# Performance work log

Measured on AMD Instinct MI355X. Metric: run time of the kernel, lower is better.

Reference implementation:

```python
import jax, jax.numpy as jnp
import numpy as np

B = 32; L = 512; D_MODEL = 512; N_LAYERS = 4
D_STATE = 64; D_CONV = 4; EXPAND = 2; HEADDIM = 64; PRED = 96
D_INNER = EXPAND * D_MODEL            # 1024
NHEADS = D_INNER // HEADDIM           # 16
CONV_DIM = D_INNER + 2 * D_STATE      # 1152
D_IN_PROJ = 2 * D_INNER + 2 * D_STATE + NHEADS  # 2192
EPS = 1e-5


def setup_inputs() -> dict:
    key = jax.random.key(0)
    ks = jax.random.split(key, 8)
    s = lambda k, shape, scale=0.02: jax.random.normal(k, shape, jnp.float32) * scale
    return {
        "x": jax.random.normal(ks[0], (B, L, D_MODEL), jnp.float32),
        "in_proj_w": s(ks[1], (N_LAYERS, D_IN_PROJ, D_MODEL)),
        "conv_w": s(ks[2], (N_LAYERS, CONV_DIM, D_CONV), 0.2),
        "conv_b": jnp.zeros((N_LAYERS, CONV_DIM), jnp.float32),
        "dt_bias": jnp.log(jnp.expm1(jax.random.uniform(ks[3], (N_LAYERS, NHEADS), minval=0.001, maxval=0.1))),
        "A_log": jnp.log(jax.random.uniform(ks[4], (N_LAYERS, NHEADS), minval=1.0, maxval=16.0)),
        "Dp": jnp.ones((N_LAYERS, NHEADS), jnp.float32),
        "norm_w": jnp.ones((N_LAYERS, D_INNER), jnp.float32),
        "out_proj_w": s(ks[5], (N_LAYERS, D_MODEL, D_INNER)),
        "ln_w": jnp.ones((N_LAYERS, D_MODEL), jnp.float32),
        "ln_b": jnp.zeros((N_LAYERS, D_MODEL), jnp.float32),
        "final_w": s(ks[6], (D_MODEL, D_MODEL)),
        "final_b": jnp.zeros((D_MODEL,), jnp.float32),
    }


def _silu(x):
    return x * jax.nn.sigmoid(x)


def _causal_dwconv(x, w, b):
    # x: (B, L, C); depthwise causal conv, kernel D_CONV, left pad D_CONV-1
    xt = jnp.swapaxes(x, 1, 2)  # (B, C, L)
    y = jax.lax.conv_general_dilated(
        xt, w[:, None, :], window_strides=(1,), padding=[(D_CONV - 1, 0)],
        feature_group_count=CONV_DIM, dimension_numbers=("NCH", "OIH", "NCH"))
    return jnp.swapaxes(y + b[None, :, None], 1, 2)


def _ssd_scan(xh, dt, Bm, Cm, A, Dp):
    # xh: (B,L,H,P), dt: (B,L,H), Bm/Cm: (B,L,N), A/Dp: (H,)
    dA = jnp.exp(dt * A)  # (B,L,H)

    def step(h, t):
        dA_t, x_t, dt_t, B_t, C_t = t  # (B,H), (B,H,P), (B,H), (B,N), (B,N)
        h = h * dA_t[:, :, None, None] + (dt_t[:, :, None] * x_t)[..., None] * B_t[:, None, None, :]
        y = jnp.einsum("bhpn,bn->bhp", h, C_t)
        return h, y

    Bb, Ll, H, P = xh.shape
    N = Bm.shape[-1]
    h0 = jnp.zeros((Bb, H, P, N), xh.dtype)
    xs = (jnp.moveaxis(dA, 1, 0), jnp.moveaxis(xh, 1, 0), jnp.moveaxis(dt, 1, 0),
          jnp.moveaxis(Bm, 1, 0), jnp.moveaxis(Cm, 1, 0))
    _, ys = jax.lax.scan(step, h0, xs)
    y = jnp.moveaxis(ys, 0, 1)  # (B,L,H,P)
    return y + xh * Dp[None, None, :, None]


def _mamba2(x, w_in, cw, cb, dtb, a_log, dp, nw, w_out):
    zxbcdt = jnp.einsum("bld,ed->ble", x, w_in)  # (B,L,D_IN_PROJ)
    z = zxbcdt[..., :D_INNER]
    xBC = zxbcdt[..., D_INNER:D_INNER + CONV_DIM]
    dt = jax.nn.softplus(zxbcdt[..., -NHEADS:] + dtb)
    xBC = _silu(_causal_dwconv(xBC, cw, cb))
    xh = xBC[..., :D_INNER].reshape(x.shape[0], x.shape[1], NHEADS, HEADDIM)
    Bm = xBC[..., D_INNER:D_INNER + D_STATE]
    Cm = xBC[..., D_INNER + D_STATE:]
    A = -jnp.exp(a_log)
    y = _ssd_scan(xh, dt, Bm, Cm, A, dp).reshape(x.shape[0], x.shape[1], D_INNER)
    # gated RMSNorm (norm_before_gate=False): gate first, then normalize
    y = y * _silu(z)
    y = y * jax.lax.rsqrt(jnp.mean(y * y, axis=-1, keepdims=True) + EPS) * nw
    return jnp.einsum("ble,de->bld", y, w_out)


def _layernorm(x, w, b):
    xc = x - jnp.mean(x, axis=-1, keepdims=True)
    return xc * jax.lax.rsqrt(jnp.mean(xc * xc, axis=-1, keepdims=True) + EPS) * w + b


def reference(x, in_proj_w, conv_w, conv_b, dt_bias, A_log, Dp, norm_w,
              out_proj_w, ln_w, ln_b, final_w, final_b):
    h = x
    for i in range(N_LAYERS):
        res = h
        h = _mamba2(h, in_proj_w[i], conv_w[i], conv_b[i], dt_bias[i],
                    A_log[i], Dp[i], norm_w[i], out_proj_w[i])
        h = _layernorm(h + res, ln_w[i], ln_b[i])
        # dropout is identity in eval mode
    h = h[:, -PRED:, :]
    return jnp.einsum("bld,ed->ble", h, final_w) + final_b
```

## Files before the change

### kernel.cpp

```cpp
#include <hip/hip_runtime.h>
#include <stdint.h>

#define BATCH 32
#define SEQ   512
#define DM    512
#define NL    4
#define DSTATE 64
#define DI    1024
#define NH    16
#define HD    64
#define PREDN 96
#define CDIM  1152
#define CSEG  144
#define DPROJ 2192
#define XBW   1168
#define NC    8
#define EPSF  1e-5f

typedef float  f32x4  __attribute__((ext_vector_type(4)));
typedef __bf16 bf16x4 __attribute__((ext_vector_type(4)));
typedef __bf16 bf16x8 __attribute__((ext_vector_type(8)));

__device__ __forceinline__ float sigmoidf_(float x){ return 1.f/(1.f+__expf(-x)); }
__device__ __forceinline__ float siluf_(float x){ return x*sigmoidf_(x); }
__device__ __forceinline__ float softplusf_(float x){ return (x>20.f)?x:log1pf(__expf(x)); }

__device__ __forceinline__ void gld16(const void* g, void* l){
  __builtin_amdgcn_global_load_lds((__attribute__((address_space(1))) void*)g,
                                   (__attribute__((address_space(3))) void*)l, 16, 0, 0);
}

template<typename TC>
__global__ __launch_bounds__(256) void gemm128(
    const __bf16* __restrict__ A, const __bf16* __restrict__ W,
    TC* __restrict__ C, TC* __restrict__ C2, const float* __restrict__ bias,
    int M, int Nreal, int ldc, int ldc2, int splitN, int K)
{
  __shared__ __bf16 sA[128*64];
  __shared__ __bf16 sW[128*64];
  const int tid  = threadIdx.x;
  const int m0   = blockIdx.y*128, n0 = blockIdx.x*128;
  const int lane = tid&63, wave = tid>>6;
  const int l15  = lane&15, quad = lane>>4;
  const int wr   = (wave>>1)*64, wc = (wave&1)*64;
  f32x4 acc[4][4];
  #pragma unroll
  for (int a=0;a<4;++a)
    #pragma unroll
    for (int b=0;b<4;++b) acc[a][b] = (f32x4){0,0,0,0};

  for (int k0=0; k0<K; k0+=64){
    #pragma unroll
    for (int j=0;j<4;++j){
      const int f = j*256 + tid;
      const int r = f>>3;
      const int kc = (((f&7) ^ (r&7)))*8;
      gld16(A + (size_t)(m0+r)*K + k0 + kc, &sA[f*8]);
      int rb = n0 + r; rb = rb < Nreal ? rb : (Nreal-1);
      gld16(W + (size_t)rb*K + k0 + kc, &sW[f*8]);
    }
    __syncthreads();
    #pragma unroll
    for (int kk=0; kk<64; kk+=32){
      const int kcb = (kk>>3) + quad;
      bf16x8 av[4], bv[4];
      #pragma unroll
      for (int mi=0;mi<4;++mi){
        const int row = wr+mi*16+l15;
        av[mi] = *(const bf16x8*)&sA[row*64 + ((kcb ^ (row&7))<<3)];
      }
      #pragma unroll
      for (int ni=0;ni<4;++ni){
        const int row = wc+ni*16+l15;
        bv[ni] = *(const bf16x8*)&sW[row*64 + ((kcb ^ (row&7))<<3)];
      }
      #pragma unroll
      for (int mi=0;mi<4;++mi)
        #pragma unroll
        for (int ni=0;ni<4;++ni)
          acc[mi][ni] = __builtin_amdgcn_mfma_f32_16x16x32_bf16(av[mi],bv[ni],acc[mi][ni],0,0,0);
    }
    __syncthreads();
  }
  #pragma unroll
  for (int ni=0;ni<4;++ni){
    const int col = n0 + wc + ni*16 + l15;
    if (col < Nreal){
      const float badd = bias ? bias[col] : 0.f;
      #pragma unroll
      for (int mi=0;mi<4;++mi){
        #pragma unroll
        for (int r4=0;r4<4;++r4){
          const int row = m0 + wr + mi*16 + quad*4 + r4;
          const float v = acc[mi][ni][r4] + badd;
          if (col < splitN) C [(size_t)row*ldc  + col]          = (TC)v;
          else              C2[(size_t)row*ldc2 + (col-splitN)] = (TC)v;
        }
      }
    }
  }
}

__global__ __launch_bounds__(256) void cast_bf16_k(
    const float* __restrict__ src, __bf16* __restrict__ dst, int n4)
{
  int i = blockIdx.x*256 + threadIdx.x;
  if (i < n4){
    float4 v = ((const float4*)src)[i];
    bf16x4 o;
    o[0]=(__bf16)v.x; o[1]=(__bf16)v.y; o[2]=(__bf16)v.z; o[3]=(__bf16)v.w;
    ((bf16x4*)dst)[i] = o;
  }
}

__global__ __launch_bounds__(256) void conv_silu_k(
    const __bf16* __restrict__ xbw, const float* __restrict__ cw,
    const float* __restrict__ cb, __bf16* __restrict__ xout,
    __bf16* __restrict__ bcout)
{
  int idx = blockIdx.x*256 + threadIdx.x;
  if (idx >= BATCH*SEQ*CSEG) return;
  const int seg = idx % CSEG;
  const int bt  = idx / CSEG;
  const int t = bt % SEQ, b = bt / SEQ;
  const int d0 = seg*8;
  const __bf16* src = xbw + ((size_t)b*SEQ + t)*XBW + d0;
  bf16x8 z8;
  #pragma unroll
  for (int e=0;e<8;++e) z8[e]=(__bf16)0.f;
  bf16x8 x3 = *(const bf16x8*)src;
  bf16x8 x2 = (t>=1)? *(const bf16x8*)(src -   XBW) : z8;
  bf16x8 x1 = (t>=2)? *(const bf16x8*)(src - 2*XBW) : z8;
  bf16x8 x0 = (t>=3)? *(const bf16x8*)(src - 3*XBW) : z8;
  const float4* w4  = (const float4*)(cw + (size_t)d0*4);
  const float4* cb4 = (const float4*)(cb + d0);
  float4 cbl = cb4[0], cbh = cb4[1];
  bf16x8 o;
  #pragma unroll
  for (int e=0;e<8;++e){
    float4 w = w4[e];
    float acc = (e<4 ? (&cbl.x)[e] : (&cbh.x)[e-4])
              + w.x*(float)x0[e] + w.y*(float)x1[e]
              + w.z*(float)x2[e] + w.w*(float)x3[e];
    o[e] = (__bf16)siluf_(acc);
  }
  if (d0 < DI) *(bf16x8*)(xout  + ((size_t)b*SEQ+t)*DI  + d0)       = o;
  else         *(bf16x8*)(bcout + ((size_t)b*SEQ+t)*128 + (d0-DI))  = o;
}

__global__ __launch_bounds__(256) void ssd_fused_k(
    const __bf16* __restrict__ bc,
    __bf16* __restrict__ xy,
    const __bf16* __restrict__ xbw,
    const float* __restrict__ dtb_, const float* __restrict__ alog_,
    const float* __restrict__ dp_)
{
  __shared__ __bf16 sB[64*72], sC[64*72], sXT[64*72], sBwT[64*72],
                    sS[64*72], sHT[64*72];
  __shared__ float sCS[SEQ], sDT[SEQ];
  const int bid = blockIdx.x;
  const int h = bid & 15, b = bid >> 4;
  const int tid = threadIdx.x, wave = tid>>6, lane = tid&63;
  const int l15 = lane&15, quad = lane>>4;
  const int wm = (wave>>1)*32, wn = (wave&1)*32;

  const float Ah  = -__expf(alog_[h]);
  const float dtb = dtb_[h];
  const float Dh  = dp_[h];

  for (int t = tid; t < SEQ; t += 256){
    float raw = (float)xbw[((size_t)b*SEQ + t)*XBW + CDIM + h];
    float dt = softplusf_(raw + dtb);
    sDT[t] = dt;
    sCS[t] = dt*Ah;
  }
  __syncthreads();
  for (int ch = wave; ch < NC; ch += 4){
    float s = sCS[ch*64 + lane];
    #pragma unroll
    for (int off=1; off<64; off<<=1){
      float v = __shfl_up(s, off);
      if (lane >= off) s += v;
    }
    sCS[ch*64 + lane] = s;
  }
  __syncthreads();

  f32x4 run[2][2];
  #pragma unroll
  for (int a=0;a<2;++a)
    #pragma unroll
    for (int d=0;d<2;++d) run[a][d] = (f32x4){0,0,0,0};

  for (int c = 0; c < NC; ++c){
    const int t0 = c*64;
    {
      const int r = tid>>2, seg = (tid&3)*16;
      const __bf16* row = bc + ((size_t)b*SEQ + t0 + r)*128;
      bf16x8 vb0 = *(const bf16x8*)(row + seg);
      bf16x8 vb1 = *(const bf16x8*)(row + seg + 8);
      bf16x8 vc0 = *(const bf16x8*)(row + 64 + seg);
      bf16x8 vc1 = *(const bf16x8*)(row + 64 + seg + 8);
      *(bf16x8*)&sB[r*72+seg]   = vb0;
      *(bf16x8*)&sB[r*72+seg+8] = vb1;
      *(bf16x8*)&sC[r*72+seg]   = vc0;
      *(bf16x8*)&sC[r*72+seg+8] = vc1;
      const float w = __expf(sCS[t0+63] - sCS[t0+r]) * sDT[t0+r];
      #pragma unroll
      for (int e=0;e<8;++e){
        sBwT[(seg+e)*72 + r]   = (__bf16)(w*(float)vb0[e]);
        sBwT[(seg+8+e)*72 + r] = (__bf16)(w*(float)vb1[e]);
      }
      const __bf16* xrow = xy + ((size_t)b*SEQ + t0 + r)*DI + h*64;
      bf16x8 vx0 = *(const bf16x8*)(xrow + seg);
      bf16x8 vx1 = *(const bf16x8*)(xrow + seg + 8);
      #pragma unroll
      for (int e=0;e<8;++e){
        sXT[(seg+e)*72 + r]   = vx0[e];
        sXT[(seg+8+e)*72 + r] = vx1[e];
      }
    }
    __syncthreads();

    f32x4 aS[2][2];
    #pragma unroll
    for (int a=0;a<2;++a)
      #pragma unroll
      for (int d=0;d<2;++d) aS[a][d] = (f32x4){0,0,0,0};
    #pragma unroll
    for (int kk=0; kk<64; kk+=32){
      const int kf = kk + quad*8;
      bf16x8 a0 = *(const bf16x8*)&sC[(wm+l15)*72+kf];
      bf16x8 a1 = *(const bf16x8*)&sC[(wm+16+l15)*72+kf];
      bf16x8 b0 = *(const bf16x8*)&sB[(wn+l15)*72+kf];
      bf16x8 b1 = *(const bf16x8*)&sB[(wn+16+l15)*72+kf];
      aS[0][0] = __builtin_amdgcn_mfma_f32_16x16x32_bf16(a0,b0,aS[0][0],0,0,0);
      aS[0][1] = __builtin_amdgcn_mfma_f32_16x16x32_bf16(a0,b1,aS[0][1],0,0,0);
      aS[1][0] = __builtin_amdgcn_mfma_f32_16x16x32_bf16(a1,b0,aS[1][0],0,0,0);
      aS[1][1] = __builtin_amdgcn_mfma_f32_16x16x32_bf16(a1,b1,aS[1][1],0,0,0);
    }
    #pragma unroll
    for (int mi=0;mi<2;++mi)
      #pragma unroll
      for (int ni=0;ni<2;++ni)
        #pragma unroll
        for (int r4=0;r4<4;++r4){
          const int i = wm+mi*16+quad*4+r4, j = wn+ni*16+l15;
          float ed = __expf(fminf(sCS[t0+i]-sCS[t0+j], 0.f)) * sDT[t0+j];
          float v = aS[mi][ni][r4]*ed;
          sS[i*72+j] = (__bf16)((j<=i)? v : 0.f);
          sHT[j*72+i] = (__bf16)run[mi][ni][r4];
        }
    __syncthreads();

    f32x4 aY[2][2], aH[2][2], aYi[2][2];
    #pragma unroll
    for (int a=0;a<2;++a)
      #pragma unroll
      for (int d=0;d<2;++d){
        aY[a][d]=(f32x4){0,0,0,0}; aH[a][d]=(f32x4){0,0,0,0};
        aYi[a][d]=(f32x4){0,0,0,0};
      }
    #pragma unroll
    for (int kk=0; kk<64; kk+=32){
      const int kf = kk + quad*8;
      bf16x8 b0 = *(const bf16x8*)&sXT[(wn+l15)*72+kf];
      bf16x8 b1 = *(const bf16x8*)&sXT[(wn+16+l15)*72+kf];
      bf16x8 s0 = *(const bf16x8*)&sS[(wm+l15)*72+kf];
      bf16x8 s1 = *(const bf16x8*)&sS[(wm+16+l15)*72+kf];
      bf16x8 w0 = *(const bf16x8*)&sBwT[(wm+l15)*72+kf];
      bf16x8 w1 = *(const bf16x8*)&sBwT[(wm+16+l15)*72+kf];
      bf16x8 c0 = *(const bf16x8*)&sC[(wm+l15)*72+kf];
      bf16x8 c1 = *(const bf16x8*)&sC[(wm+16+l15)*72+kf];
      bf16x8 h0 = *(const bf16x8*)&sHT[(wn+l15)*72+kf];
      bf16x8 h1 = *(const bf16x8*)&sHT[(wn+16+l15)*72+kf];
      aY[0][0] = __builtin_amdgcn_mfma_f32_16x16x32_bf16(s0,b0,aY[0][0],0,0,0);
      aY[0][1] = __builtin_amdgcn_mfma_f32_16x16x32_bf16(s0,b1,aY[0][1],0,0,0);
      aY[1][0] = __builtin_amdgcn_mfma_f32_16x16x32_bf16(s1,b0,aY[1][0],0,0,0);
      aY[1][1] = __builtin_amdgcn_mfma_f32_16x16x32_bf16(s1,b1,aY[1][1],0,0,0);
      aH[0][0] = __builtin_amdgcn_mfma_f32_16x16x32_bf16(w0,b0,aH[0][0],0,0,0);
      aH[0][1] = __builtin_amdgcn_mfma_f32_16x16x32_bf16(w0,b1,aH[0][1],0,0,0);
      aH[1][0] = __builtin_amdgcn_mfma_f32_16x16x32_bf16(w1,b0,aH[1][0],0,0,0);
      aH[1][1] = __builtin_amdgcn_mfma_f32_16x16x32_bf16(w1,b1,aH[1][1],0,0,0);
      aYi[0][0] = __builtin_amdgcn_mfma_f32_16x16x32_bf16(c0,h0,aYi[0][0],0,0,0);
      aYi[0][1] = __builtin_amdgcn_mfma_f32_16x16x32_bf16(c0,h1,aYi[0][1],0,0,0);
      aYi[1][0] = __builtin_amdgcn_mfma_f32_16x16x32_bf16(c1,h0,aYi[1][0],0,0,0);
      aYi[1][1] = __builtin_amdgcn_mfma_f32_16x16x32_bf16(c1,h1,aYi[1][1],0,0,0);
    }

    const float lam = __expf(sCS[t0+63]);
    #pragma unroll
    for (int mi=0;mi<2;++mi)
      #pragma unroll
      for (int ni=0;ni<2;++ni)
        #pragma unroll
        for (int r4=0;r4<4;++r4){
          const int i = wm+mi*16+quad*4+r4;
          const int p = wn+ni*16+l15;
          const float xval = (float)sXT[p*72 + i];
          const float e2 = __expf(sCS[t0+i]);
          const float yv = aY[mi][ni][r4] + Dh*xval + e2*aYi[mi][ni][r4];
          xy[((size_t)b*SEQ + t0 + i)*DI + h*64 + p] = (__bf16)yv;
          run[mi][ni][r4] = run[mi][ni][r4]*lam + aH[mi][ni][r4];
        }
    __syncthreads();
  }
}

__global__ __launch_bounds__(256) void gate_rms_k(
    __bf16* __restrict__ y, const __bf16* __restrict__ z, const float* __restrict__ nw)
{
  __shared__ float red[4];
  const int tid = threadIdx.x;
  const int sub = tid>>7;
  const int off = (tid&127)*8;
  const size_t row = (size_t)blockIdx.x*2 + sub;
  __bf16* yrow = y + row*DI;
  const __bf16* zrow = z + row*DI;
  bf16x8 yv = *(const bf16x8*)(yrow+off);
  bf16x8 zv = *(const bf16x8*)(zrow+off);
  float u[8]; float ss = 0.f;
  #pragma unroll
  for (int e=0;e<8;++e){
    float uu = (float)yv[e]*siluf_((float)zv[e]);
    u[e]=uu; ss += uu*uu;
  }
  #pragma unroll
  for (int o=32;o;o>>=1) ss += __shfl_xor(ss,o);
  if ((tid&63)==0) red[tid>>6] = ss;
  __syncthreads();
  ss = red[sub*2] + red[sub*2+1];
  const float sc = rsqrtf(ss*(1.f/DI) + EPSF);
  const float4* nw4 = (const float4*)(nw + off);
  float4 n0 = nw4[0], n1 = nw4[1];
  bf16x8 o;
  #pragma unroll
  for (int e=0;e<8;++e)
    o[e] = (__bf16)(u[e]*sc*(e<4 ? (&n0.x)[e] : (&n1.x)[e-4]));
  *(bf16x8*)(yrow+off) = o;
}

__global__ __launch_bounds__(256) void add_ln_k(
    const __bf16* __restrict__ tmp, __bf16* __restrict__ resio,
    const float* __restrict__ w, const float* __restrict__ bb)
{
  const int tid = threadIdx.x, lane = tid&63;
  const size_t row = (size_t)blockIdx.x*4 + (tid>>6);
  const int off = lane*8;
  const __bf16* trow = tmp + row*DM;
  __bf16* rrow = resio + row*DM;
  bf16x8 tv = *(const bf16x8*)(trow+off);
  bf16x8 rv = *(const bf16x8*)(rrow+off);
  float v[8]; float s = 0.f;
  #pragma unroll
  for (int e=0;e<8;++e){ v[e]=(float)tv[e]+(float)rv[e]; s += v[e]; }
  #pragma unroll
  for (int o=32;o;o>>=1) s += __shfl_xor(s,o);
  const float mean = s*(1.f/DM);
  float q = 0.f;
  #pragma unroll
  for (int e=0;e<8;++e){ v[e]-=mean; q += v[e]*v[e]; }
  #pragma unroll
  for (int o=32;o;o>>=1) q += __shfl_xor(q,o);
  const float rstd = rsqrtf(q*(1.f/DM) + EPSF);
  const float4* w4 = (const float4*)(w + off);
  const float4* b4 = (const float4*)(bb + off);
  float4 w0=w4[0], w1=w4[1], b0=b4[0], b1=b4[1];
  bf16x8 o8;
  #pragma unroll
  for (int e=0;e<8;++e){
    float we = e<4 ? (&w0.x)[e] : (&w1.x)[e-4];
    float be = e<4 ? (&b0.x)[e] : (&b1.x)[e-4];
    o8[e] = (__bf16)(v[e]*rstd*we + be);
  }
  *(bf16x8*)(rrow+off) = o8;
}

__global__ __launch_bounds__(256) void gather_k(
    const __bf16* __restrict__ xc, __bf16* __restrict__ g)
{
  int idx = blockIdx.x*256 + threadIdx.x;
  if (idx >= BATCH*PREDN*DM) return;
  int dcol = idx & (DM-1);
  int r = idx >> 9;
  int b = r / PREDN, t = (SEQ-PREDN) + (r % PREDN);
  g[idx] = xc[((size_t)b*SEQ + t)*DM + dcol];
}

extern "C" void kernel_launch(void* const* d_in, const int* in_sizes, int n_in,
                              void* d_out, int out_size, void* d_ws, size_t ws_size,
                              hipStream_t stream)
{
  const float* x         = (const float*)d_in[0];
  const float* in_proj_w = (const float*)d_in[1];
  const float* conv_w    = (const float*)d_in[2];
  const float* conv_b    = (const float*)d_in[3];
  const float* dt_bias   = (const float*)d_in[4];
  const float* A_log     = (const float*)d_in[5];
  const float* Dp        = (const float*)d_in[6];
  const float* norm_w    = (const float*)d_in[7];
  const float* out_proj_w= (const float*)d_in[8];
  const float* ln_w      = (const float*)d_in[9];
  const float* ln_b      = (const float*)d_in[10];
  const float* final_w   = (const float*)d_in[11];
  const float* final_b   = (const float*)d_in[12];
  float* out = (float*)d_out;

  const size_t ROWS = (size_t)BATCH*SEQ;
  __bf16* wbf_in  = (__bf16*)d_ws;
  __bf16* wbf_out = wbf_in  + (size_t)NL*DPROJ*DM;
  __bf16* wbf_fin = wbf_out + (size_t)NL*DM*DI;
  __bf16* zbuf    = wbf_fin + (size_t)DM*DM;
  __bf16* xbw     = zbuf    + ROWS*DI;
  __bf16* ybuf    = xbw     + ROWS*XBW;
  __bf16* bcb     = ybuf    + ROWS*DI;
  __bf16* xcur    = bcb     + ROWS*128;
  __bf16* tmp  = xbw;
  __bf16* gbuf = bcb;

  {
    int n1 = NL*DPROJ*DM/4, n2 = NL*DM*DI/4, n3 = DM*DM/4, n4 = (int)(ROWS*DM/4);
    cast_bf16_k<<<(n1+255)/256, 256, 0, stream>>>(in_proj_w,  wbf_in,  n1);
    cast_bf16_k<<<(n2+255)/256, 256, 0, stream>>>(out_proj_w, wbf_out, n2);
    cast_bf16_k<<<(n3+255)/256, 256, 0, stream>>>(final_w,    wbf_fin, n3);
    cast_bf16_k<<<(n4+255)/256, 256, 0, stream>>>(x,          xcur,    n4);
  }

  const int convTotal = BATCH*SEQ*CSEG;
  const int BIGN = 1<<30;

  for (int l=0; l<NL; ++l){
    const __bf16* wl = wbf_in + (size_t)l*DPROJ*DM;
    gemm128<__bf16><<<dim3((DPROJ+127)/128, (int)(ROWS/128)), 256, 0, stream>>>(
        xcur, wl, zbuf, xbw, nullptr, (int)ROWS, DPROJ, DI, XBW, DI, DM);
    conv_silu_k<<<(convTotal+255)/256, 256, 0, stream>>>(
        xbw, conv_w + (size_t)l*CDIM*4, conv_b + (size_t)l*CDIM, ybuf, bcb);
    ssd_fused_k<<<BATCH*NH, 256, 0, stream>>>(
        bcb, ybuf, xbw, dt_bias + l*NH, A_log + l*NH, Dp + l*NH);
    gate_rms_k<<<(int)(ROWS/2), 256, 0, stream>>>(ybuf, zbuf, norm_w + (size_t)l*DI);
    gemm128<__bf16><<<dim3(DM/128, (int)(ROWS/128)), 256, 0, stream>>>(
        ybuf, wbf_out + (size_t)l*DM*DI, tmp, tmp, nullptr, (int)ROWS, DM, DM, DM, BIGN, DI);
    add_ln_k<<<(int)(ROWS/4), 256, 0, stream>>>(tmp, xcur, ln_w + l*DM, ln_b + l*DM);
  }
  gather_k<<<(BATCH*PREDN*DM+255)/256, 256, 0, stream>>>(xcur, gbuf);
  gemm128<float><<<dim3(DM/128, (BATCH*PREDN)/128), 256, 0, stream>>>(
      gbuf, wbf_fin, out, out, final_b, BATCH*PREDN, DM, DM, DM, BIGN, DM);
}
```

Measured before the change: 893.9 us.

## Stage bf16 GEMM epilogue through LDS, fuse casts, fold gather into final GEMM

After: 866.0 us. 1.03x faster.

```diff
diff --git a/kernel.cpp b/kernel.cpp
--- a/kernel.cpp
+++ b/kernel.cpp
@@ -34,10 +34,11 @@
 __global__ __launch_bounds__(256) void gemm128(
     const __bf16* __restrict__ A, const __bf16* __restrict__ W,
     TC* __restrict__ C, TC* __restrict__ C2, const float* __restrict__ bias,
-    int M, int Nreal, int ldc, int ldc2, int splitN, int K)
-{
-  __shared__ __bf16 sA[128*64];
-  __shared__ __bf16 sW[128*64];
+    int M, int Nreal, int ldc, int ldc2, int splitN, int K, int remapA)
+{
+  __shared__ __bf16 sAB[2*128*64];
+  __bf16* sA = sAB;
+  __bf16* sW = sAB + 128*64;
   const int tid  = threadIdx.x;
   const int m0   = blockIdx.y*128, n0 = blockIdx.x*128;
   const int lane = tid&63, wave = tid>>6;
@@ -55,7 +56,9 @@
       const int f = j*256 + tid;
       const int r = f>>3;
       const int kc = (((f&7) ^ (r&7)))*8;
-      gld16(A + (size_t)(m0+r)*K + k0 + kc, &sA[f*8]);
+      int ga = m0 + r;
+      if (remapA){ int bb = ga/PREDN; ga = bb*SEQ + (SEQ-PREDN) + (ga - bb*PREDN); }
+      gld16(A + (size_t)ga*K + k0 + kc, &sA[f*8]);
       int rb = n0 + r; rb = rb < Nreal ? rb : (Nreal-1);
       gld16(W + (size_t)rb*K + k0 + kc, &sW[f*8]);
     }
@@ -82,35 +85,69 @@
     }
     __syncthreads();
   }
-  #pragma unroll
-  for (int ni=0;ni<4;++ni){
-    const int col = n0 + wc + ni*16 + l15;
-    if (col < Nreal){
-      const float badd = bias ? bias[col] : 0.f;
-      #pragma unroll
-      for (int mi=0;mi<4;++mi){
+
+  if constexpr (sizeof(TC)==2){
+    #pragma unroll
+    for (int mi=0;mi<4;++mi)
+      #pragma unroll
+      for (int ni=0;ni<4;++ni)
         #pragma unroll
         for (int r4=0;r4<4;++r4){
-          const int row = m0 + wr + mi*16 + quad*4 + r4;
-          const float v = acc[mi][ni][r4] + badd;
-          if (col < splitN) C [(size_t)row*ldc  + col]          = (TC)v;
-          else              C2[(size_t)row*ldc2 + (col-splitN)] = (TC)v;
+          const int row = wr+mi*16+quad*4+r4;
+          const int col = wc+ni*16+l15;
+          const int g2  = (col>>3) ^ (row&15);
+          sAB[row*128 + g2*8 + (col&7)] = (__bf16)acc[mi][ni][r4];
         }
-      }
-    }
-  }
-}
-
-__global__ __launch_bounds__(256) void cast_bf16_k(
-    const float* __restrict__ src, __bf16* __restrict__ dst, int n4)
+    __syncthreads();
+    #pragma unroll
+    for (int it=0; it<8; ++it){
+      const int idx = it*256 + tid;
+      const int row = idx>>4, g = idx&15;
+      const int g2 = g ^ (row&15);
+      bf16x8 v = *(const bf16x8*)&sAB[row*128 + g2*8];
+      const int col0 = n0 + g*8;
+      if (col0 < Nreal){
+        const int grow = m0 + row;
+        if (col0 < splitN) *(bf16x8*)&C [(size_t)grow*ldc  + col0]          = v;
+        else               *(bf16x8*)&C2[(size_t)grow*ldc2 + (col0-splitN)] = v;
+      }
+    }
+  } else {
+    #pragma unroll
+    for (int ni=0;ni<4;++ni){
+      const int col = n0 + wc + ni*16 + l15;
+      if (col < Nreal){
+        const float badd = bias ? bias[col] : 0.f;
+        #pragma unroll
+        for (int mi=0;mi<4;++mi){
+          #pragma unroll
+          for (int r4=0;r4<4;++r4){
+            const int row = m0 + wr + mi*16 + quad*4 + r4;
+            C[(size_t)row*ldc + col] = (TC)(acc[mi][ni][r4] + badd);
+          }
+        }
+      }
+    }
+  }
+}
+
+__global__ __launch_bounds__(256) void cast4_k(
+    const float* __restrict__ s0, __bf16* __restrict__ d0, int n0,
+    const float* __restrict__ s1, __bf16* __restrict__ d1, int n1,
+    const float* __restrict__ s2, __bf16* __restrict__ d2, int n2,
+    const float* __restrict__ s3, __bf16* __restrict__ d3, int n3)
 {
   int i = blockIdx.x*256 + threadIdx.x;
-  if (i < n4){
-    float4 v = ((const float4*)src)[i];
-    bf16x4 o;
-    o[0]=(__bf16)v.x; o[1]=(__bf16)v.y; o[2]=(__bf16)v.z; o[3]=(__bf16)v.w;
-    ((bf16x4*)dst)[i] = o;
-  }
+  const float* s; __bf16* d;
+  if (i < n0){ s=s0; d=d0; }
+  else if ((i-=n0) < n1){ s=s1; d=d1; }
+  else if ((i-=n1) < n2){ s=s2; d=d2; }
+  else if ((i-=n2) < n3){ s=s3; d=d3; }
+  else return;
+  float4 v = ((const float4*)s)[i];
+  bf16x4 o;
+  o[0]=(__bf16)v.x; o[1]=(__bf16)v.y; o[2]=(__bf16)v.z; o[3]=(__bf16)v.w;
+  ((bf16x4*)d)[i] = o;
 }
 
 __global__ __launch_bounds__(256) void conv_silu_k(
@@ -376,17 +413,6 @@
   *(bf16x8*)(rrow+off) = o8;
 }
 
-__global__ __launch_bounds__(256) void gather_k(
-    const __bf16* __restrict__ xc, __bf16* __restrict__ g)
-{
-  int idx = blockIdx.x*256 + threadIdx.x;
-  if (idx >= BATCH*PREDN*DM) return;
-  int dcol = idx & (DM-1);
-  int r = idx >> 9;
-  int b = r / PREDN, t = (SEQ-PREDN) + (r % PREDN);
-  g[idx] = xc[((size_t)b*SEQ + t)*DM + dcol];
-}
-
 extern "C" void kernel_launch(void* const* d_in, const int* in_sizes, int n_in,
                               void* d_out, int out_size, void* d_ws, size_t ws_size,
                               hipStream_t stream)
@@ -416,14 +442,13 @@
   __bf16* bcb     = ybuf    + ROWS*DI;
   __bf16* xcur    = bcb     + ROWS*128;
   __bf16* tmp  = xbw;
-  __bf16* gbuf = bcb;
 
   {
     int n1 = NL*DPROJ*DM/4, n2 = NL*DM*DI/4, n3 = DM*DM/4, n4 = (int)(ROWS*DM/4);
-    cast_bf16_k<<<(n1+255)/256, 256, 0, stream>>>(in_proj_w,  wbf_in,  n1);
-    cast_bf16_k<<<(n2+255)/256, 256, 0, stream>>>(out_proj_w, wbf_out, n2);
-    cast_bf16_k<<<(n3+255)/256, 256, 0, stream>>>(final_w,    wbf_fin, n3);
-    cast_bf16_k<<<(n4+255)/256, 256, 0, stream>>>(x,          xcur,    n4);
+    int tot = n1+n2+n3+n4;
+    cast4_k<<<(tot+255)/256, 256, 0, stream>>>(
+        in_proj_w, wbf_in, n1, out_proj_w, wbf_out, n2,
+        final_w, wbf_fin, n3, x, xcur, n4);
   }
 
   const int convTotal = BATCH*SEQ*CSEG;
@@ -432,17 +457,16 @@
   for (int l=0; l<NL; ++l){
     const __bf16* wl = wbf_in + (size_t)l*DPROJ*DM;
     gemm128<__bf16><<<dim3((DPROJ+127)/128, (int)(ROWS/128)), 256, 0, stream>>>(
-        xcur, wl, zbuf, xbw, nullptr, (int)ROWS, DPROJ, DI, XBW, DI, DM);
+        xcur, wl, zbuf, xbw, nullptr, (int)ROWS, DPROJ, DI, XBW, DI, DM, 0);
     conv_silu_k<<<(convTotal+255)/256, 256, 0, stream>>>(
         xbw, conv_w + (size_t)l*CDIM*4, conv_b + (size_t)l*CDIM, ybuf, bcb);
     ssd_fused_k<<<BATCH*NH, 256, 0, stream>>>(
         bcb, ybuf, xbw, dt_bias + l*NH, A_log + l*NH, Dp + l*NH);
     gate_rms_k<<<(int)(ROWS/2), 256, 0, stream>>>(ybuf, zbuf, norm_w + (size_t)l*DI);
     gemm128<__bf16><<<dim3(DM/128, (int)(ROWS/128)), 256, 0, stream>>>(
-        ybuf, wbf_out + (size_t)l*DM*DI, tmp, tmp, nullptr, (int)ROWS, DM, DM, DM, BIGN, DI);
+        ybuf, wbf_out + (size_t)l*DM*DI, tmp, tmp, nullptr, (int)ROWS, DM, DM, DM, BIGN, DI, 0);
     add_ln_k<<<(int)(ROWS/4), 256, 0, stream>>>(tmp, xcur, ln_w + l*DM, ln_b + l*DM);
   }
-  gather_k<<<(BATCH*PREDN*DM+255)/256, 256, 0, stream>>>(xcur, gbuf);
   gemm128<float><<<dim3(DM/128, (BATCH*PREDN)/128), 256, 0, stream>>>(
-      gbuf, wbf_fin, out, out, final_b, BATCH*PREDN, DM, DM, DM, BIGN, DM);
-}
+      xcur, wbf_fin, out, out, final_b, BATCH*PREDN, DM, DM, DM, BIGN, DM, 1);
+}
```
